# Kernel optimization log

Hardware: AMD Instinct MI355X
Metric: run time of the kernel (lower is better)

Reference implementation:

```python
import jax, jax.numpy as jnp
import numpy as np

SEQ_LEN = 8192
D_K = 128
NEG_BIG = 1000000000.0


def setup_inputs() -> dict:
    key = jax.random.key(0)
    kq, kk, kv = jax.random.split(key, 3)
    q = jax.random.normal(kq, (SEQ_LEN, D_K), dtype=jnp.float32)
    k = jax.random.normal(kk, (SEQ_LEN, D_K), dtype=jnp.float32)
    v = jax.random.normal(kv, (SEQ_LEN, D_K), dtype=jnp.float32)
    return {"q": q, "k": k, "v": v}


def reference(q, k, v):
    # q,k,v: (S, d). Naive attention with causal (look-ahead) mask, masked=True.
    d_k = q.shape[-1]
    scaled_logits = jnp.matmul(q, k.T) / jnp.sqrt(jnp.asarray(d_k, q.dtype))  # (S, S)
    look_ahead_mask = jnp.triu(jnp.ones((SEQ_LEN, SEQ_LEN), dtype=q.dtype), k=1)
    scaled_logits = scaled_logits - look_ahead_mask * NEG_BIG
    attn = jnp.matmul(jax.nn.softmax(scaled_logits, axis=-1), v)  # (S, d)
    return attn
```

## Files before the change

### kernel.cpp

```cpp
#include <hip/hip_runtime.h>
#include <hip/hip_bf16.h>
#include <math.h>

#define S_LEN 8192
#define DK    128
#define BM    64
#define BN    64
#define NQT   (S_LEN / BM)
#define SCALE 0.08838834764831845f

typedef __bf16 bf16x8_t __attribute__((ext_vector_type(8)));
typedef __bf16 bf16x4_t __attribute__((ext_vector_type(4)));
typedef float  floatx4  __attribute__((ext_vector_type(4)));

#define GLD16(g, l) __builtin_amdgcn_global_load_lds(                      \
    (const __attribute__((address_space(1))) void*)(g),                    \
    (__attribute__((address_space(3))) void*)(l), 16, 0, 0)

__global__ __launch_bounds__(256) void prep_k(const float* __restrict__ K,
                                              __bf16* __restrict__ Kb) {
  const int i = (blockIdx.x * 256 + threadIdx.x) * 4;
  float4 v = *(const float4*)&K[i];
  bf16x4_t b;
  b[0] = (__bf16)v.x; b[1] = (__bf16)v.y; b[2] = (__bf16)v.z; b[3] = (__bf16)v.w;
  *(bf16x4_t*)&Kb[i] = b;
}

__global__ __launch_bounds__(256) void prep_vt(const float* __restrict__ V,
                                               __bf16* __restrict__ Vt) {
  __shared__ __bf16 t[64][DK + 8];
  const int tid  = threadIdx.x;
  const int key0 = blockIdx.x * 64;
  {
    const int r = tid >> 2, cg = (tid & 3) * 32;
    const float* vp = V + (size_t)(key0 + r) * DK + cg;
    #pragma unroll
    for (int i = 0; i < 8; ++i) {
      float4 v = ((const float4*)vp)[i];
      bf16x4_t b;
      b[0] = (__bf16)v.x; b[1] = (__bf16)v.y; b[2] = (__bf16)v.z; b[3] = (__bf16)v.w;
      *(bf16x4_t*)&t[r][cg + i * 4] = b;
    }
  }
  __syncthreads();
  const int d = tid >> 1, h = (tid & 1) * 32;
  __bf16* op = Vt + (size_t)d * S_LEN + key0 + h;
  #pragma unroll
  for (int jb = 0; jb < 4; ++jb) {
    bf16x8_t b;
    #pragma unroll
    for (int j = 0; j < 8; ++j) b[j] = t[h + jb * 8 + j][d];
    *(bf16x8_t*)&op[jb * 8] = b;
  }
}

__global__ __launch_bounds__(256, 3)
void fa_part(const float* __restrict__ Q, const __bf16* __restrict__ Kb,
             const __bf16* __restrict__ Vtg, float* __restrict__ Opart,
             float* __restrict__ stats, int G, int direct) {
  __shared__ __align__(16) __bf16 Ks[BN * DK];
  __shared__ __align__(16) __bf16 Vts[DK * BN];
  __shared__ __align__(16) __bf16 Pl[4][16][BN + 8];

  const int tid  = threadIdx.x;
  const int wave = tid >> 6;
  const int lane = tid & 63;
  const int l15  = lane & 15;
  const int quad = lane >> 4;

  const int qtile = blockIdx.x;
  const int g     = blockIdx.y;
  const int nt    = qtile + 1;
  const int Ci    = (nt + G - 1) / G;
  const int jb0   = g * Ci;
  const int jb1   = (jb0 + Ci < nt) ? (jb0 + Ci) : nt;
  const int chunk = qtile * G + g;

  if (jb0 >= jb1) {
    if (tid < BM) {
      stats[((size_t)chunk * BM + tid) * 2 + 0] = -INFINITY;
      stats[((size_t)chunk * BM + tid) * 2 + 1] = 0.f;
    }
    return;
  }

  const int q0w = qtile * BM + wave * 16;

  bf16x8_t qf[4];
  {
    const float* qrow = Q + (size_t)(q0w + l15) * DK + quad * 8;
    #pragma unroll
    for (int kb = 0; kb < 4; ++kb) {
      const float4* p = (const float4*)(qrow + kb * 32);
      float4 a = p[0], b = p[1];
      bf16x8_t f;
      f[0]=(__bf16)a.x; f[1]=(__bf16)a.y; f[2]=(__bf16)a.z; f[3]=(__bf16)a.w;
      f[4]=(__bf16)b.x; f[5]=(__bf16)b.y; f[6]=(__bf16)b.z; f[7]=(__bf16)b.w;
      qf[kb] = f;
    }
  }

  const __bf16* kp[4]; const __bf16* vp[4];
  __bf16* kl[4]; __bf16* vl[4];
  {
    const int ck = l15 ^ ((wave * 4 + (lane >> 4)) & 15);
    const int cv = (lane & 7) ^ ((lane >> 3) & 7);
    #pragma unroll
    for (int t = 0; t < 4; ++t) {
      const int rk = t * 16 + wave * 4 + (lane >> 4);
      kp[t] = Kb + ((size_t)(jb0 * BN + rk)) * DK + ck * 8;
      kl[t] = &Ks[t * 2048 + wave * 512];
      const int rv = t * 32 + wave * 8 + (lane >> 3);
      vp[t] = Vtg + (size_t)rv * S_LEN + jb0 * BN + cv * 8;
      vl[t] = &Vts[t * 2048 + wave * 512];
    }
  }

  floatx4 o_acc[8];
  #pragma unroll
  for (int dt = 0; dt < 8; ++dt) o_acc[dt] = (floatx4){0.f, 0.f, 0.f, 0.f};
  float m_r[4], l_r[4];
  #pragma unroll
  for (int r = 0; r < 4; ++r) { m_r[r] = -INFINITY; l_r[r] = 0.f; }

  for (int jb = jb0; jb < jb1; ++jb) {
    const int key0 = jb * BN;

    #pragma unroll
    for (int t = 0; t < 4; ++t) {
      GLD16(kp[t], kl[t]);
      GLD16(vp[t], vl[t]);
      kp[t] += BN * DK;
      vp[t] += BN;
    }
    __syncthreads();

    floatx4 sv[4];
    #pragma unroll
    for (int n = 0; n < 4; ++n) {
      floatx4 acc = (floatx4){0.f, 0.f, 0.f, 0.f};
      #pragma unroll
      for (int kb = 0; kb < 4; ++kb) {
        bf16x8_t bfr = *(const bf16x8_t*)
            &Ks[(n * 16 + l15) * DK + (((kb * 4 + quad) ^ l15) * 8)];
        acc = __builtin_amdgcn_mfma_f32_16x16x32_bf16(qf[kb], bfr, acc, 0, 0, 0);
      }
      sv[n] = acc;
    }

    if (jb == qtile) {
      #pragma unroll
      for (int n = 0; n < 4; ++n) {
        const int key = key0 + n * 16 + l15;
        #pragma unroll
        for (int r = 0; r < 4; ++r) {
          const int qi = q0w + quad * 4 + r;
          float v = sv[n][r] * SCALE;
          sv[n][r] = (key > qi) ? -1e30f : v;
        }
      }
    } else {
      #pragma unroll
      for (int n = 0; n < 4; ++n)
        #pragma unroll
        for (int r = 0; r < 4; ++r) sv[n][r] *= SCALE;
    }

    float rm[4];
    #pragma unroll
    for (int r = 0; r < 4; ++r)
      rm[r] = fmaxf(fmaxf(sv[0][r], sv[1][r]), fmaxf(sv[2][r], sv[3][r]));
    #pragma unroll
    for (int off = 8; off >= 1; off >>= 1) {
      #pragma unroll
      for (int r = 0; r < 4; ++r) rm[r] = fmaxf(rm[r], __shfl_xor(rm[r], off));
    }
    float alpha[4];
    #pragma unroll
    for (int r = 0; r < 4; ++r) {
      const float mn = fmaxf(m_r[r], rm[r]);
      alpha[r] = __expf(m_r[r] - mn);
      m_r[r] = mn;
    }
    float rs[4] = {0.f, 0.f, 0.f, 0.f};
    #pragma unroll
    for (int n = 0; n < 4; ++n) {
      #pragma unroll
      for (int r = 0; r < 4; ++r) {
        const float p = __expf(sv[n][r] - m_r[r]);
        sv[n][r] = p;
        rs[r] += p;
      }
    }
    #pragma unroll
    for (int off = 8; off >= 1; off >>= 1) {
      #pragma unroll
      for (int r = 0; r < 4; ++r) rs[r] += __shfl_xor(rs[r], off);
    }
    #pragma unroll
    for (int r = 0; r < 4; ++r) l_r[r] = l_r[r] * alpha[r] + rs[r];
    #pragma unroll
    for (int dt = 0; dt < 8; ++dt)
      #pragma unroll
      for (int r = 0; r < 4; ++r) o_acc[dt][r] *= alpha[r];

    #pragma unroll
    for (int n = 0; n < 4; ++n)
      #pragma unroll
      for (int r = 0; r < 4; ++r)
        Pl[wave][quad * 4 + r][n * 16 + l15] = (__bf16)sv[n][r];
    __syncthreads();

    #pragma unroll
    for (int kc = 0; kc < 2; ++kc) {
      bf16x8_t af = *(const bf16x8_t*)&Pl[wave][l15][kc * 32 + quad * 8];
      #pragma unroll
      for (int dt = 0; dt < 8; ++dt) {
        bf16x8_t vf = *(const bf16x8_t*)
            &Vts[(dt * 16 + l15) * BN + (((kc * 4 + quad) ^ (l15 & 7)) * 8)];
        o_acc[dt] = __builtin_amdgcn_mfma_f32_16x16x32_bf16(af, vf, o_acc[dt], 0, 0, 0);
      }
    }
    __syncthreads();
  }

  if (direct) {
    #pragma unroll
    for (int r = 0; r < 4; ++r) {
      const float inv = 1.0f / l_r[r];
      float* orow = Opart + (size_t)(q0w + quad * 4 + r) * DK + l15;
      #pragma unroll
      for (int dt = 0; dt < 8; ++dt) orow[dt * 16] = o_acc[dt][r] * inv;
    }
  } else {
    #pragma unroll
    for (int r = 0; r < 4; ++r) {
      const int row = wave * 16 + quad * 4 + r;
      float* orow = Opart + ((size_t)chunk * BM + row) * DK + l15;
      #pragma unroll
      for (int dt = 0; dt < 8; ++dt) orow[dt * 16] = o_acc[dt][r];
    }
    if (l15 == 0) {
      #pragma unroll
      for (int r = 0; r < 4; ++r) {
        const int row = wave * 16 + quad * 4 + r;
        stats[((size_t)chunk * BM + row) * 2 + 0] = m_r[r];
        stats[((size_t)chunk * BM + row) * 2 + 1] = l_r[r];
      }
    }
  }
}

__global__ __launch_bounds__(256)
void fa_reduce(const float* __restrict__ Opart, const float* __restrict__ stats,
               float* __restrict__ O, int G) {
  const int wave = threadIdx.x >> 6, lane = threadIdx.x & 63;
  const int row = blockIdx.x * 4 + wave;
  const int qt = row >> 6, r = row & 63;

  float M = -INFINITY;
  for (int g = 0; g < G; ++g)
    M = fmaxf(M, stats[((size_t)(qt * G + g) * BM + r) * 2]);

  float L = 0.f;
  float ax = 0.f, ay = 0.f;
  for (int g = 0; g < G; ++g) {
    const size_t sidx = (size_t)(qt * G + g) * BM + r;
    const float m = stats[sidx * 2];
    if (m == -INFINITY) continue;
    const float w = __expf(m - M);
    L += stats[sidx * 2 + 1] * w;
    float2 o = *(const float2*)&Opart[sidx * DK + lane * 2];
    ax += w * o.x; ay += w * o.y;
  }
  const float inv = 1.f / L;
  float2 res; res.x = ax * inv; res.y = ay * inv;
  *(float2*)&O[(size_t)row * DK + lane * 2] = res;
}

extern "C" void kernel_launch(void* const* d_in, const int* in_sizes, int n_in,
                              void* d_out, int out_size, void* d_ws, size_t ws_size,
                              hipStream_t stream) {
  (void)in_sizes; (void)n_in; (void)out_size;
  const float* q = (const float*)d_in[0];
  const float* k = (const float*)d_in[1];
  const float* v = (const float*)d_in[2];
  float* out = (float*)d_out;

  const size_t conv_bytes = (size_t)S_LEN * DK * 2 * 2;
  const size_t per_g = (size_t)NQT * (BM * DK + 2 * BM) * 4;
  int G = 1;
  if (ws_size > conv_bytes + per_g) {
    G = (int)((ws_size - conv_bytes) / per_g);
    if (G > 8) G = 8;
  }

  __bf16* Kb = (__bf16*)d_ws;
  __bf16* Vt = Kb + (size_t)S_LEN * DK;
  float* Opart = (float*)(Vt + (size_t)S_LEN * DK);
  float* stats = Opart + (size_t)NQT * G * BM * DK;

  prep_k<<<(S_LEN * DK) / (256 * 4), 256, 0, stream>>>(k, Kb);
  prep_vt<<<S_LEN / 64, 256, 0, stream>>>(v, Vt);

  if (G >= 2) {
    fa_part<<<dim3(NQT, G), 256, 0, stream>>>(q, Kb, Vt, Opart, stats, G, 0);
    fa_reduce<<<S_LEN / 4, 256, 0, stream>>>(Opart, stats, out, G);
  } else {
    fa_part<<<dim3(NQT, 1), 256, 0, stream>>>(q, Kb, Vt, out, out, 1, 1);
  }
}
```

Baseline: 136.6 us.

## Use 128-row query tiles with 8 waves, fused prep kernel, bf16 partials

Doubles the query tile to 128 rows handled by 8 waves, so each K/V tile loaded into LDS is reused by twice as many query rows. Waves whose rows lie entirely before a key tile skip its compute, and the barrier between writing and reading P is removed because each wave only touches its own P slice. Q, K and the V transpose are now converted in a single fused prep kernel, and partial outputs are stored in bf16 to halve split-K traffic. The trade-offs are lower bf16 precision in the partials, idle waves on the diagonal tiles, and fewer, heavier blocks.

Result: slower. 239.7 us (+75.4%).

```diff
diff --git a/kernel.cpp b/kernel.cpp
--- a/kernel.cpp
+++ b/kernel.cpp
@@ -4,63 +4,70 @@
 
 #define S_LEN 8192
 #define DK    128
-#define BM    64
+#define BM    128
 #define BN    64
 #define NQT   (S_LEN / BM)
+#define NW    8
 #define SCALE 0.08838834764831845f
 
 typedef __bf16 bf16x8_t __attribute__((ext_vector_type(8)));
 typedef __bf16 bf16x4_t __attribute__((ext_vector_type(4)));
+typedef __bf16 bf16x2_t __attribute__((ext_vector_type(2)));
 typedef float  floatx4  __attribute__((ext_vector_type(4)));
 
 #define GLD16(g, l) __builtin_amdgcn_global_load_lds(                      \
     (const __attribute__((address_space(1))) void*)(g),                    \
     (__attribute__((address_space(3))) void*)(l), 16, 0, 0)
 
-__global__ __launch_bounds__(256) void prep_k(const float* __restrict__ K,
-                                              __bf16* __restrict__ Kb) {
-  const int i = (blockIdx.x * 256 + threadIdx.x) * 4;
-  float4 v = *(const float4*)&K[i];
-  bf16x4_t b;
-  b[0] = (__bf16)v.x; b[1] = (__bf16)v.y; b[2] = (__bf16)v.z; b[3] = (__bf16)v.w;
-  *(bf16x4_t*)&Kb[i] = b;
+__global__ __launch_bounds__(256)
+void prep(const float* __restrict__ Q, const float* __restrict__ K,
+          const float* __restrict__ V, __bf16* __restrict__ Qb,
+          __bf16* __restrict__ Kb, __bf16* __restrict__ Vt) {
+  const int b = blockIdx.x;
+  __shared__ __bf16 t[64][DK + 8];
+  if (b < 2048) {
+    const float* src = (b < 1024) ? Q : K;
+    __bf16* dst = (b < 1024) ? Qb : Kb;
+    const int i = ((b & 1023) * 256 + threadIdx.x) * 4;
+    float4 v = *(const float4*)&src[i];
+    bf16x4_t o;
+    o[0] = (__bf16)v.x; o[1] = (__bf16)v.y; o[2] = (__bf16)v.z; o[3] = (__bf16)v.w;
+    *(bf16x4_t*)&dst[i] = o;
+  } else {
+    const int tid  = threadIdx.x;
+    const int key0 = (b - 2048) * 64;
+    {
+      const int r = tid >> 2, cg = (tid & 3) * 32;
+      const float* vp = V + (size_t)(key0 + r) * DK + cg;
+      #pragma unroll
+      for (int i = 0; i < 8; ++i) {
+        float4 v = ((const float4*)vp)[i];
+        bf16x4_t o;
+        o[0]=(__bf16)v.x; o[1]=(__bf16)v.y; o[2]=(__bf16)v.z; o[3]=(__bf16)v.w;
+        *(bf16x4_t*)&t[r][cg + i * 4] = o;
+      }
+    }
+    __syncthreads();
+    const int d = tid >> 1, h = (tid & 1) * 32;
+    __bf16* op = Vt + (size_t)d * S_LEN + key0 + h;
+    #pragma unroll
+    for (int jb = 0; jb < 4; ++jb) {
+      bf16x8_t o;
+      #pragma unroll
+      for (int j = 0; j < 8; ++j) o[j] = t[h + jb * 8 + j][d];
+      *(bf16x8_t*)&op[jb * 8] = o;
+    }
+  }
 }
 
-__global__ __launch_bounds__(256) void prep_vt(const float* __restrict__ V,
-                                               __bf16* __restrict__ Vt) {
-  __shared__ __bf16 t[64][DK + 8];
-  const int tid  = threadIdx.x;
-  const int key0 = blockIdx.x * 64;
-  {
-    const int r = tid >> 2, cg = (tid & 3) * 32;
-    const float* vp = V + (size_t)(key0 + r) * DK + cg;
-    #pragma unroll
-    for (int i = 0; i < 8; ++i) {
-      float4 v = ((const float4*)vp)[i];
-      bf16x4_t b;
-      b[0] = (__bf16)v.x; b[1] = (__bf16)v.y; b[2] = (__bf16)v.z; b[3] = (__bf16)v.w;
-      *(bf16x4_t*)&t[r][cg + i * 4] = b;
-    }
-  }
-  __syncthreads();
-  const int d = tid >> 1, h = (tid & 1) * 32;
-  __bf16* op = Vt + (size_t)d * S_LEN + key0 + h;
-  #pragma unroll
-  for (int jb = 0; jb < 4; ++jb) {
-    bf16x8_t b;
-    #pragma unroll
-    for (int j = 0; j < 8; ++j) b[j] = t[h + jb * 8 + j][d];
-    *(bf16x8_t*)&op[jb * 8] = b;
-  }
-}
-
-__global__ __launch_bounds__(256, 3)
-void fa_part(const float* __restrict__ Q, const __bf16* __restrict__ Kb,
-             const __bf16* __restrict__ Vtg, float* __restrict__ Opart,
-             float* __restrict__ stats, int G, int direct) {
+__global__ __launch_bounds__(512, 6)
+void fa_part(const __bf16* __restrict__ Qb, const __bf16* __restrict__ Kb,
+             const __bf16* __restrict__ Vtg, __bf16* __restrict__ Opart,
+             float* __restrict__ Odirect, float* __restrict__ stats,
+             int G, int direct) {
   __shared__ __align__(16) __bf16 Ks[BN * DK];
   __shared__ __align__(16) __bf16 Vts[DK * BN];
-  __shared__ __align__(16) __bf16 Pl[4][16][BN + 8];
+  __shared__ __align__(16) __bf16 Pl[NW][16][BN + 8];
 
   const int tid  = threadIdx.x;
   const int wave = tid >> 6;
@@ -70,7 +77,7 @@
 
   const int qtile = blockIdx.x;
   const int g     = blockIdx.y;
-  const int nt    = qtile + 1;
+  const int nt    = 2 * qtile + 2;
   const int Ci    = (nt + G - 1) / G;
   const int jb0   = g * Ci;
   const int jb1   = (jb0 + Ci < nt) ? (jb0 + Ci) : nt;
@@ -87,33 +94,23 @@
   const int q0w = qtile * BM + wave * 16;
 
   bf16x8_t qf[4];
-  {
-    const float* qrow = Q + (size_t)(q0w + l15) * DK + quad * 8;
-    #pragma unroll
-    for (int kb = 0; kb < 4; ++kb) {
-      const float4* p = (const float4*)(qrow + kb * 32);
-      float4 a = p[0], b = p[1];
-      bf16x8_t f;
-      f[0]=(__bf16)a.x; f[1]=(__bf16)a.y; f[2]=(__bf16)a.z; f[3]=(__bf16)a.w;
-      f[4]=(__bf16)b.x; f[5]=(__bf16)b.y; f[6]=(__bf16)b.z; f[7]=(__bf16)b.w;
-      qf[kb] = f;
-    }
-  }
-
-  const __bf16* kp[4]; const __bf16* vp[4];
-  __bf16* kl[4]; __bf16* vl[4];
-  {
-    const int ck = l15 ^ ((wave * 4 + (lane >> 4)) & 15);
-    const int cv = (lane & 7) ^ ((lane >> 3) & 7);
-    #pragma unroll
-    for (int t = 0; t < 4; ++t) {
-      const int rk = t * 16 + wave * 4 + (lane >> 4);
-      kp[t] = Kb + ((size_t)(jb0 * BN + rk)) * DK + ck * 8;
-      kl[t] = &Ks[t * 2048 + wave * 512];
-      const int rv = t * 32 + wave * 8 + (lane >> 3);
-      vp[t] = Vtg + (size_t)rv * S_LEN + jb0 * BN + cv * 8;
-      vl[t] = &Vts[t * 2048 + wave * 512];
-    }
+  #pragma unroll
+  for (int kb = 0; kb < 4; ++kb)
+    qf[kb] = *(const bf16x8_t*)&Qb[(size_t)(q0w + l15) * DK + kb * 32 + quad * 8];
+
+  const __bf16* kp[2]; const __bf16* vp[2];
+  const __bf16* kl[2]; const __bf16* vl[2];
+  #pragma unroll
+  for (int t = 0; t < 2; ++t) {
+    const int s  = wave * 2 + t;
+    const int rk = 4 * s + (lane >> 4);
+    const int ck = (lane & 15) ^ (rk & 15);
+    kp[t] = Kb + ((size_t)jb0 * BN + rk) * DK + ck * 8;
+    kl[t] = Ks + s * 512;
+    const int rv = 8 * s + (lane >> 3);
+    const int cv = (lane & 7) ^ (rv & 7);
+    vp[t] = Vtg + (size_t)rv * S_LEN + jb0 * BN + cv * 8;
+    vl[t] = Vts + s * 512;
   }
 
   floatx4 o_acc[8];
@@ -127,7 +124,7 @@
     const int key0 = jb * BN;
 
     #pragma unroll
-    for (int t = 0; t < 4; ++t) {
+    for (int t = 0; t < 2; ++t) {
       GLD16(kp[t], kl[t]);
       GLD16(vp[t], vl[t]);
       kp[t] += BN * DK;
@@ -135,90 +132,91 @@
     }
     __syncthreads();
 
-    floatx4 sv[4];
-    #pragma unroll
-    for (int n = 0; n < 4; ++n) {
-      floatx4 acc = (floatx4){0.f, 0.f, 0.f, 0.f};
-      #pragma unroll
-      for (int kb = 0; kb < 4; ++kb) {
-        bf16x8_t bfr = *(const bf16x8_t*)
-            &Ks[(n * 16 + l15) * DK + (((kb * 4 + quad) ^ l15) * 8)];
-        acc = __builtin_amdgcn_mfma_f32_16x16x32_bf16(qf[kb], bfr, acc, 0, 0, 0);
-      }
-      sv[n] = acc;
-    }
-
-    if (jb == qtile) {
+    if (key0 <= q0w + 15) {
+      floatx4 sv[4];
       #pragma unroll
       for (int n = 0; n < 4; ++n) {
-        const int key = key0 + n * 16 + l15;
+        floatx4 acc = (floatx4){0.f, 0.f, 0.f, 0.f};
+        #pragma unroll
+        for (int kb = 0; kb < 4; ++kb) {
+          bf16x8_t bfr = *(const bf16x8_t*)
+              &Ks[(n * 16 + l15) * DK + (((kb * 4 + quad) ^ l15) * 8)];
+          acc = __builtin_amdgcn_mfma_f32_16x16x32_bf16(qf[kb], bfr, acc, 0, 0, 0);
+        }
+        sv[n] = acc;
+      }
+
+      if (key0 + BN - 1 > q0w) {
+        #pragma unroll
+        for (int n = 0; n < 4; ++n) {
+          const int key = key0 + n * 16 + l15;
+          #pragma unroll
+          for (int r = 0; r < 4; ++r) {
+            const int qi = q0w + quad * 4 + r;
+            float v = sv[n][r] * SCALE;
+            sv[n][r] = (key > qi) ? -1e30f : v;
+          }
+        }
+      } else {
+        #pragma unroll
+        for (int n = 0; n < 4; ++n)
+          #pragma unroll
+          for (int r = 0; r < 4; ++r) sv[n][r] *= SCALE;
+      }
+
+      float rm[4];
+      #pragma unroll
+      for (int r = 0; r < 4; ++r)
+        rm[r] = fmaxf(fmaxf(sv[0][r], sv[1][r]), fmaxf(sv[2][r], sv[3][r]));
+      #pragma unroll
+      for (int off = 8; off >= 1; off >>= 1) {
+        #pragma unroll
+        for (int r = 0; r < 4; ++r) rm[r] = fmaxf(rm[r], __shfl_xor(rm[r], off));
+      }
+      float alpha[4];
+      #pragma unroll
+      for (int r = 0; r < 4; ++r) {
+        const float mn = fmaxf(m_r[r], rm[r]);
+        alpha[r] = __expf(m_r[r] - mn);
+        m_r[r] = mn;
+      }
+      float rs[4] = {0.f, 0.f, 0.f, 0.f};
+      #pragma unroll
+      for (int n = 0; n < 4; ++n) {
         #pragma unroll
         for (int r = 0; r < 4; ++r) {
-          const int qi = q0w + quad * 4 + r;
-          float v = sv[n][r] * SCALE;
-          sv[n][r] = (key > qi) ? -1e30f : v;
+          const float p = __expf(sv[n][r] - m_r[r]);
+          sv[n][r] = p;
+          rs[r] += p;
         }
       }
-    } else {
+      #pragma unroll
+      for (int off = 8; off >= 1; off >>= 1) {
+        #pragma unroll
+        for (int r = 0; r < 4; ++r) rs[r] += __shfl_xor(rs[r], off);
+      }
+      #pragma unroll
+      for (int r = 0; r < 4; ++r) l_r[r] = l_r[r] * alpha[r] + rs[r];
+      #pragma unroll
+      for (int dt = 0; dt < 8; ++dt)
+        #pragma unroll
+        for (int r = 0; r < 4; ++r) o_acc[dt][r] *= alpha[r];
+
       #pragma unroll
       for (int n = 0; n < 4; ++n)
         #pragma unroll
-        for (int r = 0; r < 4; ++r) sv[n][r] *= SCALE;
-    }
-
-    float rm[4];
-    #pragma unroll
-    for (int r = 0; r < 4; ++r)
-      rm[r] = fmaxf(fmaxf(sv[0][r], sv[1][r]), fmaxf(sv[2][r], sv[3][r]));
-    #pragma unroll
-    for (int off = 8; off >= 1; off >>= 1) {
-      #pragma unroll
-      for (int r = 0; r < 4; ++r) rm[r] = fmaxf(rm[r], __shfl_xor(rm[r], off));
-    }
-    float alpha[4];
-    #pragma unroll
-    for (int r = 0; r < 4; ++r) {
-      const float mn = fmaxf(m_r[r], rm[r]);
-      alpha[r] = __expf(m_r[r] - mn);
-      m_r[r] = mn;
-    }
-    float rs[4] = {0.f, 0.f, 0.f, 0.f};
-    #pragma unroll
-    for (int n = 0; n < 4; ++n) {
-      #pragma unroll
-      for (int r = 0; r < 4; ++r) {
-        const float p = __expf(sv[n][r] - m_r[r]);
-        sv[n][r] = p;
-        rs[r] += p;
-      }
-    }
-    #pragma unroll
-    for (int off = 8; off >= 1; off >>= 1) {
-      #pragma unroll
-      for (int r = 0; r < 4; ++r) rs[r] += __shfl_xor(rs[r], off);
-    }
-    #pragma unroll
-    for (int r = 0; r < 4; ++r) l_r[r] = l_r[r] * alpha[r] + rs[r];
-    #pragma unroll
-    for (int dt = 0; dt < 8; ++dt)
-      #pragma unroll
-      for (int r = 0; r < 4; ++r) o_acc[dt][r] *= alpha[r];
-
-    #pragma unroll
-    for (int n = 0; n < 4; ++n)
-      #pragma unroll
-      for (int r = 0; r < 4; ++r)
-        Pl[wave][quad * 4 + r][n * 16 + l15] = (__bf16)sv[n][r];
-    __syncthreads();
-
-    #pragma unroll
-    for (int kc = 0; kc < 2; ++kc) {
-      bf16x8_t af = *(const bf16x8_t*)&Pl[wave][l15][kc * 32 + quad * 8];
-      #pragma unroll
-      for (int dt = 0; dt < 8; ++dt) {
-        bf16x8_t vf = *(const bf16x8_t*)
-            &Vts[(dt * 16 + l15) * BN + (((kc * 4 + quad) ^ (l15 & 7)) * 8)];
-        o_acc[dt] = __builtin_amdgcn_mfma_f32_16x16x32_bf16(af, vf, o_acc[dt], 0, 0, 0);
+        for (int r = 0; r < 4; ++r)
+          Pl[wave][quad * 4 + r][n * 16 + l15] = (__bf16)sv[n][r];
+
+      #pragma unroll
+      for (int kc = 0; kc < 2; ++kc) {
+        bf16x8_t af = *(const bf16x8_t*)&Pl[wave][l15][kc * 32 + quad * 8];
+        #pragma unroll
+        for (int dt = 0; dt < 8; ++dt) {
+          bf16x8_t vf = *(const bf16x8_t*)
+              &Vts[(dt * 16 + l15) * BN + (((kc * 4 + quad) ^ (l15 & 7)) * 8)];
+          o_acc[dt] = __builtin_amdgcn_mfma_f32_16x16x32_bf16(af, vf, o_acc[dt], 0, 0, 0);
+        }
       }
     }
     __syncthreads();
@@ -228,7 +226,7 @@
     #pragma unroll
     for (int r = 0; r < 4; ++r) {
       const float inv = 1.0f / l_r[r];
-      float* orow = Opart + (size_t)(q0w + quad * 4 + r) * DK + l15;
+      float* orow = Odirect + (size_t)(q0w + quad * 4 + r) * DK + l15;
       #pragma unroll
       for (int dt = 0; dt < 8; ++dt) orow[dt * 16] = o_acc[dt][r] * inv;
     }
@@ -236,9 +234,9 @@
     #pragma unroll
     for (int r = 0; r < 4; ++r) {
       const int row = wave * 16 + quad * 4 + r;
-      float* orow = Opart + ((size_t)chunk * BM + row) * DK + l15;
-      #pragma unroll
-      for (int dt = 0; dt < 8; ++dt) orow[dt * 16] = o_acc[dt][r];
+      __bf16* orow = Opart + ((size_t)chunk * BM + row) * DK + l15;
+      #pragma unroll
+      for (int dt = 0; dt < 8; ++dt) orow[dt * 16] = (__bf16)o_acc[dt][r];
     }
     if (l15 == 0) {
       #pragma unroll
@@ -252,26 +250,26 @@
 }
 
 __global__ __launch_bounds__(256)
-void fa_reduce(const float* __restrict__ Opart, const float* __restrict__ stats,
+void fa_reduce(const __bf16* __restrict__ Opart, const float* __restrict__ stats,
                float* __restrict__ O, int G) {
   const int wave = threadIdx.x >> 6, lane = threadIdx.x & 63;
   const int row = blockIdx.x * 4 + wave;
-  const int qt = row >> 6, r = row & 63;
+  const int qt = row >> 7, r = row & 127;
 
   float M = -INFINITY;
   for (int g = 0; g < G; ++g)
     M = fmaxf(M, stats[((size_t)(qt * G + g) * BM + r) * 2]);
 
-  float L = 0.f;
-  float ax = 0.f, ay = 0.f;
+  float L = 0.f, ax = 0.f, ay = 0.f;
   for (int g = 0; g < G; ++g) {
     const size_t sidx = (size_t)(qt * G + g) * BM + r;
     const float m = stats[sidx * 2];
     if (m == -INFINITY) continue;
     const float w = __expf(m - M);
     L += stats[sidx * 2 + 1] * w;
-    float2 o = *(const float2*)&Opart[sidx * DK + lane * 2];
-    ax += w * o.x; ay += w * o.y;
+    bf16x2_t o = *(const bf16x2_t*)&Opart[sidx * DK + lane * 2];
+    ax += w * (float)o[0];
+    ay += w * (float)o[1];
   }
   const float inv = 1.f / L;
   float2 res; res.x = ax * inv; res.y = ay * inv;
@@ -287,26 +285,27 @@
   const float* v = (const float*)d_in[2];
   float* out = (float*)d_out;
 
-  const size_t conv_bytes = (size_t)S_LEN * DK * 2 * 2;
-  const size_t per_g = (size_t)NQT * (BM * DK + 2 * BM) * 4;
+  const size_t conv = 3 * (size_t)S_LEN * DK * 2;
+  const size_t per_g = (size_t)NQT * BM * DK * 2
+                     + (size_t)NQT * BM * 2 * sizeof(float);
   int G = 1;
-  if (ws_size > conv_bytes + per_g) {
-    G = (int)((ws_size - conv_bytes) / per_g);
+  if (ws_size > conv + 2 * per_g) {
+    G = (int)((ws_size - conv) / per_g);
     if (G > 8) G = 8;
   }
 
-  __bf16* Kb = (__bf16*)d_ws;
+  __bf16* Qb = (__bf16*)d_ws;
+  __bf16* Kb = Qb + (size_t)S_LEN * DK;
   __bf16* Vt = Kb + (size_t)S_LEN * DK;
-  float* Opart = (float*)(Vt + (size_t)S_LEN * DK);
-  float* stats = Opart + (size_t)NQT * G * BM * DK;
-
-  prep_k<<<(S_LEN * DK) / (256 * 4), 256, 0, stream>>>(k, Kb);
-  prep_vt<<<S_LEN / 64, 256, 0, stream>>>(v, Vt);
+  __bf16* Opart = Vt + (size_t)S_LEN * DK;
+  float* stats = (float*)(Opart + (size_t)NQT * G * BM * DK);
+
+  prep<<<2176, 256, 0, stream>>>(q, k, v, Qb, Kb, Vt);
 
   if (G >= 2) {
-    fa_part<<<dim3(NQT, G), 256, 0, stream>>>(q, Kb, Vt, Opart, stats, G, 0);
+    fa_part<<<dim3(NQT, G), 512, 0, stream>>>(Qb, Kb, Vt, Opart, nullptr, stats, G, 0);
     fa_reduce<<<S_LEN / 4, 256, 0, stream>>>(Opart, stats, out, G);
   } else {
-    fa_part<<<dim3(NQT, 1), 256, 0, stream>>>(q, Kb, Vt, out, out, 1, 1);
+    fa_part<<<dim3(NQT, 1), 512, 0, stream>>>(Qb, Kb, Vt, Opart, out, stats, 1, 1);
   }
 }
```
